# Optimization experiments

Hardware: AMD Instinct MI355X
Metric: run time of the kernel (lower is better)

The kernel has to match this reference:

```python
import jax, jax.numpy as jnp
import numpy as np

B, L, D, DFF, MODES = 16, 1536, 512, 2048, 64
KERNELS = (3, 5, 7)


def setup_inputs() -> dict:
    key = jax.random.key(0)
    ks = jax.random.split(key, 12)
    scale = 1.0 / (D * D)
    f32 = jnp.float32
    return {
        "x": jax.random.normal(ks[0], (B, L, D), f32),
        "w_real": scale * jax.random.normal(ks[1], (D, D, MODES), f32),
        "w_imag": scale * jax.random.normal(ks[2], (D, D, MODES), f32),
        "conv1_w": jax.random.normal(ks[3], (DFF, D), f32) / np.sqrt(D).astype(np.float32),
        "conv2_w": jax.random.normal(ks[4], (D, DFF), f32) / np.sqrt(DFF).astype(np.float32),
        "d1_w1": jax.random.normal(ks[5], (D // 2, D), f32) / np.sqrt(D).astype(np.float32),
        "d1_b1": jnp.zeros((D // 2,), f32),
        "d1_w2": jax.random.normal(ks[6], (len(KERNELS), D // 2), f32) / np.sqrt(D // 2).astype(np.float32),
        "d1_b2": jnp.zeros((len(KERNELS),), f32),
        "d2_w1": jax.random.normal(ks[7], (D // 2, D), f32) / np.sqrt(D).astype(np.float32),
        "d2_b1": jnp.zeros((D // 2,), f32),
        "d2_w2": jax.random.normal(ks[8], (len(KERNELS), D // 2), f32) / np.sqrt(D // 2).astype(np.float32),
        "d2_b2": jnp.zeros((len(KERNELS),), f32),
    }


def _avg_pool1d(x, k):
    # torch AvgPool1d(kernel=k, stride=1, padding=k//2), count_include_pad=True:
    # zero-pad then divide by k everywhere. x: (B, L, D) -> (B, L, D) for odd k.
    pad = k // 2
    xp = jnp.pad(x, ((0, 0), (pad, pad), (0, 0)))
    cs = jnp.pad(jnp.cumsum(xp, axis=1), ((0, 0), (1, 0), (0, 0)))
    return (cs[:, k:, :] - cs[:, :-k, :]) / k


def _moe_decomp(x, w1, b1, w2, b2):
    # trends: (B, L, D, E)
    trends = jnp.stack([_avg_pool1d(x, k) for k in KERNELS], axis=-1)
    h = jax.nn.relu(jnp.einsum("bld,hd->blh", x, w1) + b1)
    logits = jnp.einsum("blh,eh->ble", h, w2) + b2
    gates = jax.nn.softmax(logits, axis=-1)[:, :, None, :]  # (B, L, 1, E)
    x_trend = jnp.sum(trends * gates, axis=-1)
    return x - x_trend  # seasonal component


def _fourier_block(x, w_real, w_imag):
    q_ft = jnp.fft.rfft(x, axis=1)  # (B, L//2+1, D) complex
    modes = min(MODES, q_ft.shape[1])
    weights = (w_real + 1j * w_imag).astype(jnp.complex64)  # (D, D, modes)
    # batched complex matmul over the kept modes (fuses the per-mode loop)
    out_m = jnp.einsum("bmd,dem->bme", q_ft[:, :modes, :], weights[:, :, :modes])
    out_ft = jnp.zeros((x.shape[0], x.shape[1] // 2 + 1, x.shape[2]), jnp.complex64)
    out_ft = out_ft.at[:, :modes, :].set(out_m)
    return jnp.fft.irfft(out_ft, n=x.shape[1], axis=1)


def reference(x, w_real, w_imag, conv1_w, conv2_w,
              d1_w1, d1_b1, d1_w2, d1_b2,
              d2_w1, d2_b1, d2_w2, d2_b2):
    # FEB-f + residual (dropout = identity in eval)
    x = x + _fourier_block(x, w_real, w_imag)
    x = _moe_decomp(x, d1_w1, d1_b1, d1_w2, d1_b2)
    # 1x1 conv FFN == per-token linear layers
    y = jax.nn.relu(jnp.einsum("bld,fd->blf", x, conv1_w))
    y = jnp.einsum("blf,df->bld", y, conv2_w)
    res = _moe_decomp(x + y, d2_w1, d2_b1, d2_w2, d2_b2)
    return res
```

## Files before the change

### kernel.cpp

```cpp
#include <hip/hip_runtime.h>

#define B_   16
#define L_   1536
#define D_   512
#define DFF_ 2048
#define NM   64
#define HID  256

typedef short short8  __attribute__((ext_vector_type(8)));
typedef short short4v __attribute__((ext_vector_type(4)));
typedef float f32x4   __attribute__((ext_vector_type(4)));

__device__ __forceinline__ float b2f(short s) {
  unsigned int u = ((unsigned int)(unsigned short)s) << 16;
  float f; __builtin_memcpy(&f, &u, 4); return f;
}
__device__ __forceinline__ short f2b(float f) {
  unsigned int u; __builtin_memcpy(&u, &f, 4);
  u += 0x7fffu + ((u >> 16) & 1u);
  return (short)(u >> 16);
}
__device__ __forceinline__ f32x4 zero4() {
  f32x4 v; v[0]=0.f; v[1]=0.f; v[2]=0.f; v[3]=0.f; return v;
}

#define MFMA(a,b,c) __builtin_amdgcn_mfma_f32_16x16x32_bf16((a),(b),(c),0,0,0)
#define SWZ(row, grp) (((row) << 6) + ((((grp) ^ ((row) & 7))) << 3))

__global__ __launch_bounds__(256) void zero_out(float* __restrict__ o, int n) {
  int i = blockIdx.x * 256 + threadIdx.x;
  if (i < n) o[i] = 0.f;
}

__global__ __launch_bounds__(256) void cvt_f32_bf16(const float* __restrict__ s,
                                                    short* __restrict__ d, int n4) {
  int i = blockIdx.x * 256 + threadIdx.x;
  if (i >= n4) return;
  f32x4 v = ((const f32x4*)s)[i];
  short4v o;
  #pragma unroll
  for (int j = 0; j < 4; ++j) o[j] = f2b(v[j]);
  ((short4v*)d)[i] = o;
}

__global__ __launch_bounds__(256) void build_fwd_tables(short* __restrict__ tc,
                                                        short* __restrict__ ts) {
  int i = blockIdx.x * 256 + threadIdx.x;
  if (i >= NM * L_) return;
  int m = i / L_, l = i - m * L_;
  int r = (m * l) % L_;
  float th = (float)r * (6.283185307179586f / (float)L_);
  float s, c; __sincosf(th, &s, &c);
  tc[i] = f2b(c);
  ts[i] = f2b(-s);
}
__global__ __launch_bounds__(256) void build_basis(short* __restrict__ basis) {
  int i = blockIdx.x * 256 + threadIdx.x;
  if (i >= L_ * 128) return;
  int l = i >> 7, k = i & 127;
  int m = (k < 64) ? k : (k - 64);
  int r = (m * l) % L_;
  float th = (float)r * (6.283185307179586f / (float)L_);
  float s, c; __sincosf(th, &s, &c);
  float v = (k < 64) ? ((m == 0) ? 1.f : 2.f) * (1.f / (float)L_) * c
                     : (-2.f / (float)L_) * s;
  basis[i] = f2b(v);
}

__global__ __launch_bounds__(256) void transpose_w16(const float* __restrict__ w,
                                                     short* __restrict__ wt, int mBase) {
  __shared__ float tile[64][17];
  int dc = blockIdx.x, e = blockIdx.y, t = threadIdx.x;
  {
    int dl = t >> 2, mg = t & 3;
    f32x4 v = *(const f32x4*)(w + ((long)(dc * 64 + dl) * 512 + e) * 64 + mBase + mg * 4);
    tile[dl][mg*4+0] = v[0]; tile[dl][mg*4+1] = v[1];
    tile[dl][mg*4+2] = v[2]; tile[dl][mg*4+3] = v[3];
  }
  __syncthreads();
  if (t < 128) {
    int mr = t >> 3, dg = t & 7;
    short8 o;
    #pragma unroll
    for (int j = 0; j < 8; ++j) o[j] = f2b(tile[dg * 8 + j][mr]);
    *(short8*)(wt + ((long)mr * 512 + e) * 512 + dc * 64 + dg * 8) = o;
  }
}

__global__ __launch_bounds__(256) void transpose_x(const float* __restrict__ x,
                                                   short* __restrict__ xt) {
  __shared__ float tile[64][65];
  int dc = blockIdx.x, lc = blockIdx.y, b = blockIdx.z, t = threadIdx.x;
  const float* xb = x + (long)b * L_ * D_;
  #pragma unroll
  for (int i = 0; i < 4; ++i) {
    int idx = i * 256 + t; int ll = idx >> 4, dg = idx & 15;
    f32x4 v = *(const f32x4*)(xb + (long)(lc * 64 + ll) * D_ + dc * 64 + dg * 4);
    tile[ll][dg*4+0] = v[0]; tile[ll][dg*4+1] = v[1];
    tile[ll][dg*4+2] = v[2]; tile[ll][dg*4+3] = v[3];
  }
  __syncthreads();
  #pragma unroll
  for (int i = 0; i < 2; ++i) {
    int idx = i * 256 + t; int dl = idx >> 3, lg = idx & 7;
    short8 o;
    #pragma unroll
    for (int j = 0; j < 8; ++j) o[j] = f2b(tile[lg * 8 + j][dl]);
    *(short8*)(xt + ((long)b * D_ + dc * 64 + dl) * L_ + lc * 64 + lg * 8) = o;
  }
}

template<bool RELU, bool HASBIAS, bool HASRES, bool RESB, bool OUTB>
__global__ __launch_bounds__(256) void gemm64(
    const short* __restrict__ A, long ldA, long Az,
    const short* __restrict__ W, long ldW, long Wz,
    const float* __restrict__ bias,
    const void* __restrict__ res, long ldres, long resZ,
    short* __restrict__ outB,
    long csr, long csc, long csz, int K)
{
  __shared__ short lA[64 * 64];
  __shared__ short lW[64 * 64];
  const int t = threadIdx.x;
  const int lane = t & 63, wid = t >> 6;
  const int quad = lane >> 4, l15 = lane & 15;
  const int wm = (wid & 1) * 32, wn = (wid >> 1) * 32;
  const long row0 = (long)blockIdx.x * 64;
  const long col0 = (long)blockIdx.y * 64;
  const int z = blockIdx.z;
  const short* Ab = A + (long)z * Az + row0 * ldA;
  const short* Wb = W + (long)z * Wz + col0 * ldW;

  f32x4 acc[2][2];
  #pragma unroll
  for (int i = 0; i < 2; ++i)
    #pragma unroll
    for (int j = 0; j < 2; ++j) acc[i][j] = zero4();

  for (int k0 = 0; k0 < K; k0 += 64) {
    __syncthreads();
    #pragma unroll
    for (int i = 0; i < 2; ++i) {
      int idx = i * 256 + t;
      int r = idx >> 3, cg = idx & 7;
      *(short8*)&lA[SWZ(r, cg)] = *(const short8*)(Ab + (long)r * ldA + k0 + cg * 8);
      *(short8*)&lW[SWZ(r, cg)] = *(const short8*)(Wb + (long)r * ldW + k0 + cg * 8);
    }
    __syncthreads();
    #pragma unroll
    for (int ks = 0; ks < 2; ++ks) {
      int gq = ks * 4 + quad;
      short8 a0 = *(const short8*)&lA[SWZ(wm + l15, gq)];
      short8 a1 = *(const short8*)&lA[SWZ(wm + 16 + l15, gq)];
      short8 b0 = *(const short8*)&lW[SWZ(wn + l15, gq)];
      short8 b1 = *(const short8*)&lW[SWZ(wn + 16 + l15, gq)];
      acc[0][0] = MFMA(a0, b0, acc[0][0]);
      acc[0][1] = MFMA(a0, b1, acc[0][1]);
      acc[1][0] = MFMA(a1, b0, acc[1][0]);
      acc[1][1] = MFMA(a1, b1, acc[1][1]);
    }
  }
  #pragma unroll
  for (int ni = 0; ni < 2; ++ni) {
    long col = col0 + wn + ni * 16 + l15;
    float bv = HASBIAS ? bias[col] : 0.f;
    #pragma unroll
    for (int mi = 0; mi < 2; ++mi) {
      #pragma unroll
      for (int r = 0; r < 4; ++r) {
        long row = row0 + wm + mi * 16 + quad * 4 + r;
        float v = acc[mi][ni][r];
        if (HASBIAS) v += bv;
        if (RELU)    v = fmaxf(v, 0.f);
        if (HASRES) {
          long ro = (long)z * resZ + row * ldres + col;
          v += RESB ? b2f(((const short*)res)[ro]) : ((const float*)res)[ro];
        }
        outB[(long)z * csz + row * csr + col * csc] = f2b(v);
      }
    }
  }
}

__global__ __launch_bounds__(256) void mode_gemm(
    const short* __restrict__ qr, const short* __restrict__ qi,
    const short* __restrict__ wr, const short* __restrict__ wi,
    short* __restrict__ outm, int mBase)
{
  __shared__ short lqr[16 * 64], lqi[16 * 64], lwr[64 * 64], lwi[64 * 64];
  const int ml = blockIdx.x, en = blockIdx.y;
  const int m = mBase + ml;
  const int t = threadIdx.x, lane = t & 63, wid = t >> 6;
  const int quad = lane >> 4, l15 = lane & 15;
  const short* qrb = qr + (long)m * (B_ * D_);
  const short* qib = qi + (long)m * (B_ * D_);
  const short* wrb = wr + (long)ml * (D_ * D_) + (long)en * 64 * D_;
  const short* wib = wi + (long)ml * (D_ * D_) + (long)en * 64 * D_;
  f32x4 accr = zero4(), acci = zero4();
  for (int k0 = 0; k0 < D_; k0 += 64) {
    __syncthreads();
    {
      int idx = t & 127; int r = idx >> 3, cg = idx & 7;
      const short* src = (t < 128 ? qrb : qib) + r * D_ + k0 + cg * 8;
      short* dst = (t < 128) ? lqr : lqi;
      *(short8*)&dst[SWZ(r, cg)] = *(const short8*)src;
    }
    #pragma unroll
    for (int i = 0; i < 4; ++i) {
      int idx = i * 256 + t;
      int which = idx >> 9, idx2 = idx & 511;
      int r = idx2 >> 3, cg = idx2 & 7;
      const short* src = (which ? wib : wrb) + r * D_ + k0 + cg * 8;
      short* dst = which ? lwi : lwr;
      *(short8*)&dst[SWZ(r, cg)] = *(const short8*)src;
    }
    __syncthreads();
    #pragma unroll
    for (int ks = 0; ks < 2; ++ks) {
      int gq = ks * 4 + quad;
      short8 ar = *(const short8*)&lqr[SWZ(l15, gq)];
      short8 ai = *(const short8*)&lqi[SWZ(l15, gq)];
      short8 br = *(const short8*)&lwr[SWZ(wid * 16 + l15, gq)];
      short8 bi = *(const short8*)&lwi[SWZ(wid * 16 + l15, gq)];
      short8 nai;
      #pragma unroll
      for (int j = 0; j < 8; ++j) nai[j] = (short)(ai[j] ^ (short)0x8000);
      accr = MFMA(ar, br, accr);
      accr = MFMA(nai, bi, accr);
      acci = MFMA(ar, bi, acci);
      acci = MFMA(ai, br, acci);
    }
  }
  #pragma unroll
  for (int r = 0; r < 4; ++r) {
    int bb = quad * 4 + r;
    long e = (long)en * 64 + wid * 16 + l15;
    long base = ((long)bb * D_ + e) * 128 + m;
    outm[base]      = f2b(accr[r]);
    outm[base + 64] = f2b(acci[r]);
  }
}

__global__ __launch_bounds__(256) void gates_kernel(
    const short* __restrict__ h, const float* __restrict__ w2,
    const float* __restrict__ b2, float* __restrict__ g, int rows)
{
  int wid = threadIdx.x >> 6, lane = threadIdx.x & 63;
  int row = blockIdx.x * 4 + wid;
  if (row >= rows) return;
  const short* hr = h + (long)row * HID;
  short4v hh = *(const short4v*)(hr + lane * 4);
  float hv[4];
  #pragma unroll
  for (int j = 0; j < 4; ++j) hv[j] = b2f(hh[j]);
  float lg[3];
  #pragma unroll
  for (int e = 0; e < 3; ++e) {
    const float* wrow = w2 + e * HID + lane * 4;
    float p = hv[0] * wrow[0] + hv[1] * wrow[1] + hv[2] * wrow[2] + hv[3] * wrow[3];
    #pragma unroll
    for (int off = 32; off >= 1; off >>= 1) p += __shfl_xor(p, off);
    lg[e] = p + b2[e];
  }
  float mx = fmaxf(lg[0], fmaxf(lg[1], lg[2]));
  float e0 = __expf(lg[0] - mx), e1 = __expf(lg[1] - mx), e2 = __expf(lg[2] - mx);
  float inv = 1.f / (e0 + e1 + e2);
  float gv = (lane == 0) ? e0 * inv : (lane == 1) ? e1 * inv : e2 * inv;
  if (lane < 3) g[(long)row * 3 + lane] = gv;
}

template<bool OUTF, bool WRITEB>
__global__ __launch_bounds__(512) void combine_kernel(
    const short* __restrict__ xin, const float* __restrict__ g,
    float* __restrict__ outf, short* __restrict__ outb)
{
  int lc = blockIdx.x, b = blockIdx.y, d = threadIdx.x;
  int l0 = lc * 64;
  const short* xb = xin + (long)b * L_ * D_ + d;
  const float* gb = g + (long)b * L_ * 3;
  float win[7];
  #pragma unroll
  for (int j = 0; j < 6; ++j) {
    int l = l0 - 3 + j;
    win[j] = (l >= 0 && l < L_) ? b2f(xb[(long)l * D_]) : 0.f;
  }
  for (int i = 0; i < 64; ++i) {
    int lcn = l0 + i;
    int lr = lcn + 3;
    win[6] = (lr < L_) ? b2f(xb[(long)lr * D_]) : 0.f;
    float s3 = win[2] + win[3] + win[4];
    float s5 = s3 + win[1] + win[5];
    float s7 = s5 + win[0] + win[6];
    float g0 = gb[lcn * 3 + 0], g1 = gb[lcn * 3 + 1], g2 = gb[lcn * 3 + 2];
    float trend = g0 * s3 * (1.f / 3.f) + g1 * s5 * (1.f / 5.f) + g2 * s7 * (1.f / 7.f);
    float v = win[3] - trend;
    long o = ((long)b * L_ + lcn) * D_ + d;
    if (OUTF)   outf[o] = v;
    if (WRITEB) outb[o] = f2b(v);
    #pragma unroll
    for (int j = 0; j < 6; ++j) win[j] = win[j + 1];
  }
}

extern "C" void kernel_launch(void* const* d_in, const int* in_sizes, int n_in,
                              void* d_out, int out_size, void* d_ws, size_t ws_size,
                              hipStream_t stream) {
  const float* x       = (const float*)d_in[0];
  const float* w_real  = (const float*)d_in[1];
  const float* w_imag  = (const float*)d_in[2];
  const float* conv1_w = (const float*)d_in[3];
  const float* conv2_w = (const float*)d_in[4];
  const float* d1_w1   = (const float*)d_in[5];
  const float* d1_b1   = (const float*)d_in[6];
  const float* d1_w2   = (const float*)d_in[7];
  const float* d1_b2   = (const float*)d_in[8];
  const float* d2_w1   = (const float*)d_in[9];
  const float* d2_b1   = (const float*)d_in[10];
  const float* d2_w2   = (const float*)d_in[11];
  const float* d2_b2   = (const float*)d_in[12];
  float* OUT = (float*)d_out;

  const size_t REQUIRED = 115343360;
  if (ws_size < REQUIRED) {
    zero_out<<<(out_size + 255) / 256, 256, 0, stream>>>(OUT, out_size);
    return;
  }

  char* ws = (char*)d_ws;
  short* C1WB  = (short*)(ws + 0);
  short* C2WB  = (short*)(ws + 2097152);
  short* D1W1B = (short*)(ws + 4194304);
  short* D2W1B = (short*)(ws + 4456448);
  short* TC    = (short*)(ws + 4718592);
  short* TS    = (short*)(ws + 4915200);
  short* BASIS = (short*)(ws + 5111808);
  float* G     = (float*)(ws + 5505024);
  short* XT    = (short*)(ws + 6291456);
  short* Y1C   = XT;
  short* QR    = (short*)(ws + 31457280);
  short* QI    = (short*)(ws + 32505856);
  short* OUTM  = (short*)(ws + 33554432);
  short* WCR   = (short*)(ws + 35651584);
  short* WCI   = (short*)(ws + 44040192);
  short* X1B   = (short*)(ws + 52428800);
  short* ZB    = X1B;
  short* X2B   = (short*)(ws + 77594624);
  short* H     = (short*)(ws + 102760448);

  cvt_f32_bf16<<<(262144 + 255) / 256, 256, 0, stream>>>(conv1_w, C1WB, 262144);
  cvt_f32_bf16<<<(262144 + 255) / 256, 256, 0, stream>>>(conv2_w, C2WB, 262144);
  cvt_f32_bf16<<<(32768 + 255) / 256, 256, 0, stream>>>(d1_w1, D1W1B, 32768);
  cvt_f32_bf16<<<(32768 + 255) / 256, 256, 0, stream>>>(d2_w1, D2W1B, 32768);
  build_fwd_tables<<<(NM * L_ + 255) / 256, 256, 0, stream>>>(TC, TS);
  build_basis<<<(L_ * 128 + 255) / 256, 256, 0, stream>>>(BASIS);
  transpose_x<<<dim3(8, 24, 16), 256, 0, stream>>>(x, XT);

  gemm64<false, false, false, false, true><<<dim3(8, 1, 16), 256, 0, stream>>>(
      XT, L_, (long)D_ * L_, TC, L_, 0, nullptr, nullptr, 0, 0,
      QR, 1, (long)B_ * D_, D_, L_);
  gemm64<false, false, false, false, true><<<dim3(8, 1, 16), 256, 0, stream>>>(
      XT, L_, (long)D_ * L_, TS, L_, 0, nullptr, nullptr, 0, 0,
      QI, 1, (long)B_ * D_, D_, L_);

  for (int c = 0; c < 4; ++c) {
    transpose_w16<<<dim3(8, 512), 256, 0, stream>>>(w_real, WCR, c * 16);
    transpose_w16<<<dim3(8, 512), 256, 0, stream>>>(w_imag, WCI, c * 16);
    mode_gemm<<<dim3(16, 8), 256, 0, stream>>>(QR, QI, WCR, WCI, OUTM, c * 16);
  }

  gemm64<false, false, true, false, true><<<dim3(24, 8, 16), 256, 0, stream>>>(
      BASIS, 128, 0, OUTM, 128, (long)D_ * 128, nullptr,
      x, D_, (long)L_ * D_, X1B, D_, 1, (long)L_ * D_, 128);

  gemm64<true, true, false, false, true><<<dim3(384, 4, 1), 256, 0, stream>>>(
      X1B, D_, 0, D1W1B, D_, 0, d1_b1, nullptr, 0, 0,
      H, HID, 1, 0, D_);
  gates_kernel<<<6144, 256, 0, stream>>>(H, d1_w2, d1_b2, G, B_ * L_);
  combine_kernel<false, true><<<dim3(24, 16), 512, 0, stream>>>(X1B, G, nullptr, X2B);

  for (int rc = 0; rc < 4; ++rc) {
    const short* Ain = X2B + (long)rc * 6144 * D_;
    gemm64<true, false, false, false, true><<<dim3(96, 32, 1), 256, 0, stream>>>(
        Ain, D_, 0, C1WB, D_, 0, nullptr, nullptr, 0, 0,
        Y1C, DFF_, 1, 0, D_);
    gemm64<false, false, true, true, true><<<dim3(96, 8, 1), 256, 0, stream>>>(
        Y1C, DFF_, 0, C2WB, DFF_, 0, nullptr, Ain, D_, 0,
        ZB + (long)rc * 6144 * D_, D_, 1, 0, DFF_);
  }

  gemm64<true, true, false, false, true><<<dim3(384, 4, 1), 256, 0, stream>>>(
      ZB, D_, 0, D2W1B, D_, 0, d2_b1, nullptr, 0, 0,
      H, HID, 1, 0, D_);
  gates_kernel<<<6144, 256, 0, stream>>>(H, d2_w2, d2_b2, G, B_ * L_);
  combine_kernel<true, false><<<dim3(24, 16), 512, 0, stream>>>(ZB, G, OUT, nullptr);
}
```

Baseline: 680.6 us.

## Use 128x128 GEMM tiles with direct global-to-LDS loads and merge DFT/mode launches

Replaces the 64x64 GEMM with a 128x128-tile kernel in which each wave computes a 4x4 grid of MFMA tiles and fills LDS through global_load_lds with the swizzle folded into the source addresses. The forward DFT becomes a single GEMM against a combined cos/sin table, followed by a transpose into the mode-major layout. The weight transposes and the mode GEMM are each issued as one launch over all 64 modes instead of four chunks. This cuts LDS traffic per MFMA and launch count, at the cost of more registers per thread, fewer blocks on the small GEMMs, and reuse of workspace buffers.

Measured after the change: 699.6 us. +2.8%, slower.

```diff
diff --git a/kernel.cpp b/kernel.cpp
--- a/kernel.cpp
+++ b/kernel.cpp
@@ -26,6 +26,9 @@
 
 #define MFMA(a,b,c) __builtin_amdgcn_mfma_f32_16x16x32_bf16((a),(b),(c),0,0,0)
 #define SWZ(row, grp) (((row) << 6) + ((((grp) ^ ((row) & 7))) << 3))
+#define GLDS16(gp, lp) __builtin_amdgcn_global_load_lds( \
+    (const __attribute__((address_space(1))) void*)(gp), \
+    (__attribute__((address_space(3))) void*)(lp), 16, 0, 0)
 
 __global__ __launch_bounds__(256) void zero_out(float* __restrict__ o, int n) {
   int i = blockIdx.x * 256 + threadIdx.x;
@@ -43,16 +46,15 @@
   ((short4v*)d)[i] = o;
 }
 
-__global__ __launch_bounds__(256) void build_fwd_tables(short* __restrict__ tc,
-                                                        short* __restrict__ ts) {
+__global__ __launch_bounds__(256) void build_tcs(short* __restrict__ tcs) {
   int i = blockIdx.x * 256 + threadIdx.x;
-  if (i >= NM * L_) return;
+  if (i >= 128 * L_) return;
   int m = i / L_, l = i - m * L_;
-  int r = (m * l) % L_;
+  int mm = (m < 64) ? m : (m - 64);
+  int r = (mm * l) % L_;
   float th = (float)r * (6.283185307179586f / (float)L_);
   float s, c; __sincosf(th, &s, &c);
-  tc[i] = f2b(c);
-  ts[i] = f2b(-s);
+  tcs[i] = f2b((m < 64) ? c : -s);
 }
 __global__ __launch_bounds__(256) void build_basis(short* __restrict__ basis) {
   int i = blockIdx.x * 256 + threadIdx.x;
@@ -67,10 +69,11 @@
   basis[i] = f2b(v);
 }
 
-__global__ __launch_bounds__(256) void transpose_w16(const float* __restrict__ w,
-                                                     short* __restrict__ wt, int mBase) {
+__global__ __launch_bounds__(256) void transpose_w(const float* __restrict__ w,
+                                                   short* __restrict__ wt) {
   __shared__ float tile[64][17];
   int dc = blockIdx.x, e = blockIdx.y, t = threadIdx.x;
+  int mBase = blockIdx.z * 16;
   {
     int dl = t >> 2, mg = t & 3;
     f32x4 v = *(const f32x4*)(w + ((long)(dc * 64 + dl) * 512 + e) * 64 + mBase + mg * 4);
@@ -83,7 +86,7 @@
     short8 o;
     #pragma unroll
     for (int j = 0; j < 8; ++j) o[j] = f2b(tile[dg * 8 + j][mr]);
-    *(short8*)(wt + ((long)mr * 512 + e) * 512 + dc * 64 + dg * 8) = o;
+    *(short8*)(wt + ((long)(mBase + mr) * 512 + e) * 512 + dc * 64 + dg * 8) = o;
   }
 }
 
@@ -110,73 +113,103 @@
   }
 }
 
-template<bool RELU, bool HASBIAS, bool HASRES, bool RESB, bool OUTB>
-__global__ __launch_bounds__(256) void gemm64(
+__global__ __launch_bounds__(256) void transpose_q(const short* __restrict__ in,
+                                                   short* __restrict__ out) {
+  __shared__ short tile[64][72];
+  int ct = blockIdx.x, rt = blockIdx.y, t = threadIdx.x;
+  int r0 = rt * 64, c0 = ct * 64;
+  #pragma unroll
+  for (int i = 0; i < 2; ++i) {
+    int idx = i * 256 + t; int r = idx >> 3, g = idx & 7;
+    short8 v = *(const short8*)(in + (long)(r0 + r) * 128 + c0 + g * 8);
+    #pragma unroll
+    for (int j = 0; j < 8; ++j) tile[r][g * 8 + j] = v[j];
+  }
+  __syncthreads();
+  #pragma unroll
+  for (int i = 0; i < 2; ++i) {
+    int idx = i * 256 + t; int c = idx >> 3, g = idx & 7;
+    short8 o;
+    #pragma unroll
+    for (int j = 0; j < 8; ++j) o[j] = tile[g * 8 + j][c];
+    *(short8*)(out + (long)(c0 + c) * 8192 + r0 + g * 8) = o;
+  }
+}
+
+template<bool RELU, bool HASBIAS, bool HASRES, bool RESB>
+__global__ __launch_bounds__(256) void gemm128(
     const short* __restrict__ A, long ldA, long Az,
     const short* __restrict__ W, long ldW, long Wz,
     const float* __restrict__ bias,
     const void* __restrict__ res, long ldres, long resZ,
-    short* __restrict__ outB,
-    long csr, long csc, long csz, int K)
+    short* __restrict__ outB, long ldC, long Cz, int K)
 {
-  __shared__ short lA[64 * 64];
-  __shared__ short lW[64 * 64];
-  const int t = threadIdx.x;
-  const int lane = t & 63, wid = t >> 6;
+  __shared__ short lA[128 * 64];
+  __shared__ short lW[128 * 64];
+  const int t = threadIdx.x, lane = t & 63, wid = t >> 6;
   const int quad = lane >> 4, l15 = lane & 15;
-  const int wm = (wid & 1) * 32, wn = (wid >> 1) * 32;
-  const long row0 = (long)blockIdx.x * 64;
-  const long col0 = (long)blockIdx.y * 64;
+  const int wm = (wid & 1) * 64, wn = (wid >> 1) * 64;
+  const long row0 = (long)blockIdx.x * 128, col0 = (long)blockIdx.y * 128;
   const int z = blockIdx.z;
   const short* Ab = A + (long)z * Az + row0 * ldA;
   const short* Wb = W + (long)z * Wz + col0 * ldW;
 
-  f32x4 acc[2][2];
-  #pragma unroll
-  for (int i = 0; i < 2; ++i)
-    #pragma unroll
-    for (int j = 0; j < 2; ++j) acc[i][j] = zero4();
+  int srcrow[4]; long srcoff[4];
+  #pragma unroll
+  for (int i = 0; i < 4; ++i) {
+    int c = wid * 4 + i;
+    int r = c * 8 + (lane >> 3);
+    int g = (lane & 7) ^ (r & 7);
+    srcrow[i] = r; srcoff[i] = g * 8;
+  }
+
+  f32x4 acc[4][4];
+  #pragma unroll
+  for (int i = 0; i < 4; ++i)
+    #pragma unroll
+    for (int j = 0; j < 4; ++j) acc[i][j] = zero4();
 
   for (int k0 = 0; k0 < K; k0 += 64) {
     __syncthreads();
     #pragma unroll
-    for (int i = 0; i < 2; ++i) {
-      int idx = i * 256 + t;
-      int r = idx >> 3, cg = idx & 7;
-      *(short8*)&lA[SWZ(r, cg)] = *(const short8*)(Ab + (long)r * ldA + k0 + cg * 8);
-      *(short8*)&lW[SWZ(r, cg)] = *(const short8*)(Wb + (long)r * ldW + k0 + cg * 8);
+    for (int i = 0; i < 4; ++i) {
+      int c = wid * 4 + i;
+      GLDS16(Ab + (long)srcrow[i] * ldA + k0 + srcoff[i], lA + c * 512);
+      GLDS16(Wb + (long)srcrow[i] * ldW + k0 + srcoff[i], lW + c * 512);
     }
     __syncthreads();
     #pragma unroll
     for (int ks = 0; ks < 2; ++ks) {
       int gq = ks * 4 + quad;
-      short8 a0 = *(const short8*)&lA[SWZ(wm + l15, gq)];
-      short8 a1 = *(const short8*)&lA[SWZ(wm + 16 + l15, gq)];
-      short8 b0 = *(const short8*)&lW[SWZ(wn + l15, gq)];
-      short8 b1 = *(const short8*)&lW[SWZ(wn + 16 + l15, gq)];
-      acc[0][0] = MFMA(a0, b0, acc[0][0]);
-      acc[0][1] = MFMA(a0, b1, acc[0][1]);
-      acc[1][0] = MFMA(a1, b0, acc[1][0]);
-      acc[1][1] = MFMA(a1, b1, acc[1][1]);
-    }
-  }
-  #pragma unroll
-  for (int ni = 0; ni < 2; ++ni) {
+      short8 av[4], bv[4];
+      #pragma unroll
+      for (int mi = 0; mi < 4; ++mi) av[mi] = *(const short8*)&lA[SWZ(wm + mi * 16 + l15, gq)];
+      #pragma unroll
+      for (int ni = 0; ni < 4; ++ni) bv[ni] = *(const short8*)&lW[SWZ(wn + ni * 16 + l15, gq)];
+      #pragma unroll
+      for (int mi = 0; mi < 4; ++mi)
+        #pragma unroll
+        for (int ni = 0; ni < 4; ++ni)
+          acc[mi][ni] = MFMA(av[mi], bv[ni], acc[mi][ni]);
+    }
+  }
+  #pragma unroll
+  for (int ni = 0; ni < 4; ++ni) {
     long col = col0 + wn + ni * 16 + l15;
-    float bv = HASBIAS ? bias[col] : 0.f;
-    #pragma unroll
-    for (int mi = 0; mi < 2; ++mi) {
+    float bvv = HASBIAS ? bias[col] : 0.f;
+    #pragma unroll
+    for (int mi = 0; mi < 4; ++mi) {
       #pragma unroll
       for (int r = 0; r < 4; ++r) {
         long row = row0 + wm + mi * 16 + quad * 4 + r;
         float v = acc[mi][ni][r];
-        if (HASBIAS) v += bv;
+        if (HASBIAS) v += bvv;
         if (RELU)    v = fmaxf(v, 0.f);
         if (HASRES) {
           long ro = (long)z * resZ + row * ldres + col;
           v += RESB ? b2f(((const short*)res)[ro]) : ((const float*)res)[ro];
         }
-        outB[(long)z * csz + row * csr + col * csc] = f2b(v);
+        outB[(long)z * Cz + row * ldC + col] = f2b(v);
       }
     }
   }
@@ -185,17 +218,16 @@
 __global__ __launch_bounds__(256) void mode_gemm(
     const short* __restrict__ qr, const short* __restrict__ qi,
     const short* __restrict__ wr, const short* __restrict__ wi,
-    short* __restrict__ outm, int mBase)
+    short* __restrict__ outm)
 {
   __shared__ short lqr[16 * 64], lqi[16 * 64], lwr[64 * 64], lwi[64 * 64];
-  const int ml = blockIdx.x, en = blockIdx.y;
-  const int m = mBase + ml;
+  const int m = blockIdx.x, en = blockIdx.y;
   const int t = threadIdx.x, lane = t & 63, wid = t >> 6;
   const int quad = lane >> 4, l15 = lane & 15;
   const short* qrb = qr + (long)m * (B_ * D_);
   const short* qib = qi + (long)m * (B_ * D_);
-  const short* wrb = wr + (long)ml * (D_ * D_) + (long)en * 64 * D_;
-  const short* wib = wi + (long)ml * (D_ * D_) + (long)en * 64 * D_;
+  const short* wrb = wr + (long)m * (D_ * D_) + (long)en * 64 * D_;
+  const short* wib = wi + (long)m * (D_ * D_) + (long)en * 64 * D_;
   f32x4 accr = zero4(), acci = zero4();
   for (int k0 = 0; k0 < D_; k0 += 64) {
     __syncthreads();
@@ -320,7 +352,7 @@
   const float* d2_b2   = (const float*)d_in[12];
   float* OUT = (float*)d_out;
 
-  const size_t REQUIRED = 115343360;
+  const size_t REQUIRED = 106954752;
   if (ws_size < REQUIRED) {
     zero_out<<<(out_size + 255) / 256, 256, 0, stream>>>(OUT, out_size);
     return;
@@ -331,66 +363,57 @@
   short* C2WB  = (short*)(ws + 2097152);
   short* D1W1B = (short*)(ws + 4194304);
   short* D2W1B = (short*)(ws + 4456448);
-  short* TC    = (short*)(ws + 4718592);
-  short* TS    = (short*)(ws + 4915200);
+  short* TCS   = (short*)(ws + 4718592);
   short* BASIS = (short*)(ws + 5111808);
   float* G     = (float*)(ws + 5505024);
   short* XT    = (short*)(ws + 6291456);
+  short* QRI   = XT;
   short* Y1C   = XT;
-  short* QR    = (short*)(ws + 31457280);
-  short* QI    = (short*)(ws + 32505856);
+  short* QT    = (short*)(ws + 31457280);
+  short* ZB    = QT;
   short* OUTM  = (short*)(ws + 33554432);
-  short* WCR   = (short*)(ws + 35651584);
-  short* WCI   = (short*)(ws + 44040192);
-  short* X1B   = (short*)(ws + 52428800);
-  short* ZB    = X1B;
-  short* X2B   = (short*)(ws + 77594624);
-  short* H     = (short*)(ws + 102760448);
+  short* WTR   = (short*)(ws + 35651584);
+  short* X1B   = WTR;
+  short* WTI   = (short*)(ws + 69206016);
+  short* X2B   = WTI;
+  short* H     = (short*)(ws + 94371840);
 
   cvt_f32_bf16<<<(262144 + 255) / 256, 256, 0, stream>>>(conv1_w, C1WB, 262144);
   cvt_f32_bf16<<<(262144 + 255) / 256, 256, 0, stream>>>(conv2_w, C2WB, 262144);
   cvt_f32_bf16<<<(32768 + 255) / 256, 256, 0, stream>>>(d1_w1, D1W1B, 32768);
   cvt_f32_bf16<<<(32768 + 255) / 256, 256, 0, stream>>>(d2_w1, D2W1B, 32768);
-  build_fwd_tables<<<(NM * L_ + 255) / 256, 256, 0, stream>>>(TC, TS);
+  build_tcs<<<(128 * L_ + 255) / 256, 256, 0, stream>>>(TCS);
   build_basis<<<(L_ * 128 + 255) / 256, 256, 0, stream>>>(BASIS);
+  transpose_w<<<dim3(8, 512, 4), 256, 0, stream>>>(w_real, WTR);
+  transpose_w<<<dim3(8, 512, 4), 256, 0, stream>>>(w_imag, WTI);
   transpose_x<<<dim3(8, 24, 16), 256, 0, stream>>>(x, XT);
 
-  gemm64<false, false, false, false, true><<<dim3(8, 1, 16), 256, 0, stream>>>(
-      XT, L_, (long)D_ * L_, TC, L_, 0, nullptr, nullptr, 0, 0,
-      QR, 1, (long)B_ * D_, D_, L_);
-  gemm64<false, false, false, false, true><<<dim3(8, 1, 16), 256, 0, stream>>>(
-      XT, L_, (long)D_ * L_, TS, L_, 0, nullptr, nullptr, 0, 0,
-      QI, 1, (long)B_ * D_, D_, L_);
-
-  for (int c = 0; c < 4; ++c) {
-    transpose_w16<<<dim3(8, 512), 256, 0, stream>>>(w_real, WCR, c * 16);
-    transpose_w16<<<dim3(8, 512), 256, 0, stream>>>(w_imag, WCI, c * 16);
-    mode_gemm<<<dim3(16, 8), 256, 0, stream>>>(QR, QI, WCR, WCI, OUTM, c * 16);
-  }
-
-  gemm64<false, false, true, false, true><<<dim3(24, 8, 16), 256, 0, stream>>>(
+  gemm128<false, false, false, false><<<dim3(64, 1, 1), 256, 0, stream>>>(
+      XT, L_, 0, TCS, L_, 0, nullptr, nullptr, 0, 0, QT, 128, 0, L_);
+  transpose_q<<<dim3(2, 128), 256, 0, stream>>>(QT, QRI);
+
+  mode_gemm<<<dim3(64, 8), 256, 0, stream>>>(QRI, QRI + 64 * B_ * D_, WTR, WTI, OUTM);
+
+  gemm128<false, false, true, false><<<dim3(12, 4, 16), 256, 0, stream>>>(
       BASIS, 128, 0, OUTM, 128, (long)D_ * 128, nullptr,
-      x, D_, (long)L_ * D_, X1B, D_, 1, (long)L_ * D_, 128);
-
-  gemm64<true, true, false, false, true><<<dim3(384, 4, 1), 256, 0, stream>>>(
-      X1B, D_, 0, D1W1B, D_, 0, d1_b1, nullptr, 0, 0,
-      H, HID, 1, 0, D_);
+      x, D_, (long)L_ * D_, X1B, D_, (long)L_ * D_, 128);
+
+  gemm128<true, true, false, false><<<dim3(192, 2, 1), 256, 0, stream>>>(
+      X1B, D_, 0, D1W1B, D_, 0, d1_b1, nullptr, 0, 0, H, HID, 0, D_);
   gates_kernel<<<6144, 256, 0, stream>>>(H, d1_w2, d1_b2, G, B_ * L_);
   combine_kernel<false, true><<<dim3(24, 16), 512, 0, stream>>>(X1B, G, nullptr, X2B);
 
   for (int rc = 0; rc < 4; ++rc) {
     const short* Ain = X2B + (long)rc * 6144 * D_;
-    gemm64<true, false, false, false, true><<<dim3(96, 32, 1), 256, 0, stream>>>(
-        Ain, D_, 0, C1WB, D_, 0, nullptr, nullptr, 0, 0,
-        Y1C, DFF_, 1, 0, D_);
-    gemm64<false, false, true, true, true><<<dim3(96, 8, 1), 256, 0, stream>>>(
+    gemm128<true, false, false, false><<<dim3(48, 16, 1), 256, 0, stream>>>(
+        Ain, D_, 0, C1WB, D_, 0, nullptr, nullptr, 0, 0, Y1C, DFF_, 0, D_);
+    gemm128<false, false, true, true><<<dim3(48, 4, 1), 256, 0, stream>>>(
         Y1C, DFF_, 0, C2WB, DFF_, 0, nullptr, Ain, D_, 0,
-        ZB + (long)rc * 6144 * D_, D_, 1, 0, DFF_);
-  }
-
-  gemm64<true, true, false, false, true><<<dim3(384, 4, 1), 256, 0, stream>>>(
-      ZB, D_, 0, D2W1B, D_, 0, d2_b1, nullptr, 0, 0,
-      H, HID, 1, 0, D_);
+        ZB + (long)rc * 6144 * D_, D_, 0, DFF_);
+  }
+
+  gemm128<true, true, false, false><<<dim3(192, 2, 1), 256, 0, stream>>>(
+      ZB, D_, 0, D2W1B, D_, 0, d2_b1, nullptr, 0, 0, H, HID, 0, D_);
   gates_kernel<<<6144, 256, 0, stream>>>(H, d2_w2, d2_b2, G, B_ * L_);
   combine_kernel<true, false><<<dim3(24, 16), 512, 0, stream>>>(ZB, G, OUT, nullptr);
 }
```
